# Performance work log

Measured on AMD Instinct MI355X. Metric: run time of the kernel, lower is better.

## Reference

```python
import jax, jax.numpy as jnp
import numpy as np

HIDDEN = 2048
N_HEADS = 16
N_KV_HEADS = 8
HEAD_DIM = 128
ROTARY_DIM = 32  # int(128 * 0.25), already even
ROPE_THETA = 10000000.0
EPS = 1e-6
BATCH, SEQ = 2, 2048


def _rmsnorm(x, w, eps=EPS):
    # per-head RMSNorm over last dim; weight is zero-init, scale = 1 + w
    r = jax.lax.rsqrt(jnp.mean(x * x, axis=-1, keepdims=True) + eps)
    return x * r * (1.0 + w)


def _rope(x, positions, rotary_dim, theta):
    # x: [b, s, h, rotary_dim]; rotate-halves RoPE
    half = rotary_dim // 2
    inv_freq = 1.0 / (theta ** (jnp.arange(half, dtype=jnp.float32) / half))
    ang = positions.astype(jnp.float32)[:, :, None] * inv_freq  # [b, s, half]
    cos = jnp.cos(ang)[:, :, None, :]
    sin = jnp.sin(ang)[:, :, None, :]
    x1, x2 = x[..., :half], x[..., half:]
    return jnp.concatenate([x1 * cos - x2 * sin, x1 * sin + x2 * cos], axis=-1)


def setup_inputs() -> dict:
    key = jax.random.key(0)
    ks = jax.random.split(key, 8)
    scale = lambda fan_in: 1.0 / np.sqrt(fan_in)
    x = jax.random.normal(ks[0], (BATCH, SEQ, HIDDEN), dtype=jnp.float32)
    Wq = jax.random.normal(ks[1], (HIDDEN, N_HEADS * HEAD_DIM * 2), jnp.float32) * scale(HIDDEN)
    Wk = jax.random.normal(ks[2], (HIDDEN, N_KV_HEADS * HEAD_DIM), jnp.float32) * scale(HIDDEN)
    Wv = jax.random.normal(ks[3], (HIDDEN, N_KV_HEADS * HEAD_DIM), jnp.float32) * scale(HIDDEN)
    Wo = jax.random.normal(ks[4], (N_HEADS * HEAD_DIM, HIDDEN), jnp.float32) * scale(N_HEADS * HEAD_DIM)
    q_norm_w = jax.random.normal(ks[5], (HEAD_DIM,), jnp.float32) * 0.02
    k_norm_w = jax.random.normal(ks[6], (HEAD_DIM,), jnp.float32) * 0.02
    attention_mask = jnp.ones((BATCH, SEQ), dtype=jnp.int32)
    positions = jnp.broadcast_to(jnp.arange(SEQ, dtype=jnp.int32), (BATCH, SEQ))
    return {"x": x, "attention_mask": attention_mask, "positions": positions,
            "Wq": Wq, "Wk": Wk, "Wv": Wv, "Wo": Wo,
            "q_norm_w": q_norm_w, "k_norm_w": k_norm_w}


def reference(x, attention_mask, positions, Wq, Wk, Wv, Wo, q_norm_w, k_norm_w):
    b, s, _ = x.shape
    g = N_HEADS // N_KV_HEADS  # GQA group size

    q_all = jnp.einsum('bsh,ho->bso', x, Wq).reshape(b, s, N_HEADS, HEAD_DIM * 2)
    q, gate = jnp.split(q_all, 2, axis=-1)          # each [b,s,H,D]
    gate = gate.reshape(b, s, N_HEADS * HEAD_DIM)
    q = _rmsnorm(q, q_norm_w)
    k = _rmsnorm(jnp.einsum('bsh,ho->bso', x, Wk).reshape(b, s, N_KV_HEADS, HEAD_DIM), k_norm_w)
    v = jnp.einsum('bsh,ho->bso', x, Wv).reshape(b, s, N_KV_HEADS, HEAD_DIM)

    # partial RoPE on first ROTARY_DIM dims
    q = jnp.concatenate([_rope(q[..., :ROTARY_DIM], positions, ROTARY_DIM, ROPE_THETA), q[..., ROTARY_DIM:]], axis=-1)
    k = jnp.concatenate([_rope(k[..., :ROTARY_DIM], positions, ROTARY_DIM, ROPE_THETA), k[..., ROTARY_DIM:]], axis=-1)

    # grouped-query causal attention
    qg = q.reshape(b, s, N_KV_HEADS, g, HEAD_DIM)
    scores = jnp.einsum('bqhgd,bkhd->bhgqk', qg, k) / jnp.sqrt(jnp.float32(HEAD_DIM))
    causal = jnp.tril(jnp.ones((s, s), dtype=bool))
    key_valid = attention_mask.astype(bool)[:, None, None, None, :]  # [b,1,1,1,k]
    mask = causal[None, None, None, :, :] & key_valid
    scores = jnp.where(mask, scores, jnp.finfo(scores.dtype).min)
    probs = jax.nn.softmax(scores, axis=-1)
    attn = jnp.einsum('bhgqk,bkhd->bqhgd', probs, v).reshape(b, s, N_HEADS * HEAD_DIM)

    attn = attn * jax.nn.sigmoid(gate)
    return jnp.einsum('bso,oh->bsh', attn, Wo)
```

## Files before the change

### kernel.cpp

```cpp
#include <hip/hip_runtime.h>
#include <cstdint>

typedef __bf16  bf16;
typedef __bf16  bf16x8 __attribute__((ext_vector_type(8)));
typedef __bf16  bf16x4 __attribute__((ext_vector_type(4)));
typedef float   f32x4  __attribute__((ext_vector_type(4)));

#define GLOAD_LDS16(g, l) __builtin_amdgcn_global_load_lds( \
    (const __attribute__((address_space(1))) void*)(g),     \
    (__attribute__((address_space(3))) void*)(l), 16, 0, 0)

#define SEQ   2048
#define HID   2048
#define NH    16
#define NKV   8
#define HD    128
#define NQKV  6144
#define MTOT  4096

__global__ __launch_bounds__(256) void convx(const float* __restrict__ x, bf16* __restrict__ xb) {
    int i = blockIdx.x * 256 + threadIdx.x;
    f32x4 v = ((const f32x4*)x)[i];
    bf16x4 o;
    o[0] = (bf16)v[0]; o[1] = (bf16)v[1]; o[2] = (bf16)v[2]; o[3] = (bf16)v[3];
    ((bf16x4*)xb)[i] = o;
}

__global__ __launch_bounds__(256) void transw(const float* __restrict__ W, bf16* __restrict__ WT, int N) {
    int n0 = blockIdx.x * 64, k0 = blockIdx.y * 64;
    __shared__ float tile[64][65];
    int t = threadIdx.x;
    int tn = t & 63, t4 = t >> 6;
    #pragma unroll
    for (int i = 0; i < 16; ++i) {
        int kk = i * 4 + t4;
        tile[kk][tn] = W[(size_t)(k0 + kk) * N + n0 + tn];
    }
    __syncthreads();
    #pragma unroll
    for (int i = 0; i < 16; ++i) {
        int nn = i * 4 + t4;
        WT[(size_t)(n0 + nn) * HID + k0 + tn] = (bf16)tile[tn][nn];
    }
}

template<bool OUT_BF16>
__global__ __launch_bounds__(256) void gemm_bt(const bf16* __restrict__ A, const bf16* __restrict__ Bt,
                                               void* __restrict__ C, int M, int N, int K) {
    __shared__ __align__(16) bf16 As[128 * 32];
    __shared__ __align__(16) bf16 Bs[128 * 32];
    const int tid = threadIdx.x;
    const int wave = tid >> 6, lane = tid & 63;
    const int quad = lane >> 4, cl = lane & 15;
    const int tile_n = blockIdx.x * 128, tile_m = blockIdx.y * 128;
    const int wm = (wave & 1) * 64, wn = (wave >> 1) * 64;
    f32x4 acc[4][4] = {};

    for (int k0 = 0; k0 < K; k0 += 32) {
        #pragma unroll
        for (int j = 0; j < 2; ++j) {
            int c = (j * 4 + wave) * 64 + lane;
            int row = c >> 2, kq = c & 3;
            GLOAD_LDS16(A  + (size_t)(tile_m + row) * K + k0 + kq * 8, As + (size_t)(j * 4 + wave) * 512);
            GLOAD_LDS16(Bt + (size_t)(tile_n + row) * K + k0 + kq * 8, Bs + (size_t)(j * 4 + wave) * 512);
        }
        __syncthreads();
        bf16x8 a[4], b[4];
        #pragma unroll
        for (int t = 0; t < 4; ++t) {
            a[t] = *(const bf16x8*)(As + (wm + t * 16 + cl) * 32 + quad * 8);
            b[t] = *(const bf16x8*)(Bs + (wn + t * 16 + cl) * 32 + quad * 8);
        }
        #pragma unroll
        for (int mt = 0; mt < 4; ++mt)
            #pragma unroll
            for (int nt = 0; nt < 4; ++nt)
                acc[mt][nt] = __builtin_amdgcn_mfma_f32_16x16x32_bf16(a[mt], b[nt], acc[mt][nt], 0, 0, 0);
        __syncthreads();
    }
    #pragma unroll
    for (int mt = 0; mt < 4; ++mt)
        #pragma unroll
        for (int nt = 0; nt < 4; ++nt)
            #pragma unroll
            for (int r = 0; r < 4; ++r) {
                int row = tile_m + wm + mt * 16 + quad * 4 + r;
                int col = tile_n + wn + nt * 16 + cl;
                float v = acc[mt][nt][r];
                if (OUT_BF16) ((bf16*)C)[(size_t)row * N + col] = (bf16)v;
                else          ((float*)C)[(size_t)row * N + col] = v;
            }
}

__global__ __launch_bounds__(256) void qk_post(const bf16* __restrict__ qkv,
                                               const float* __restrict__ qnw, const float* __restrict__ knw,
                                               const int* __restrict__ positions,
                                               bf16* __restrict__ Qh, bf16* __restrict__ Kh) {
    int tk = blockIdx.x;
    int b = tk >> 11, s = tk & 2047;
    int wave = threadIdx.x >> 6, lane = threadIdx.x & 63;
    float pos = (float)positions[tk];
    int fi = lane & 15;
    float ang = pos * exp2f(-(float)fi * 1.4533435415278355f);
    float cv = cosf(ang), sv = sinf(ang);

    #pragma unroll
    for (int i = 0; i < 4; ++i) {
        int h = wave + i * 4;
        const bf16* base = qkv + (size_t)tk * NQKV + h * 256;
        float v0 = (float)base[lane], v1 = (float)base[lane + 64];
        float ssq = v0 * v0 + v1 * v1;
        #pragma unroll
        for (int off = 32; off; off >>= 1) ssq += __shfl_xor(ssq, off);
        float rn = rsqrtf(ssq * (1.0f / 128.0f) + 1e-6f);
        float q0 = v0 * rn * (1.0f + qnw[lane]);
        float q1 = v1 * rn * (1.0f + qnw[lane + 64]);
        float other = __shfl_xor(q0, 16);
        float q0r = q0;
        if (lane < 16)      q0r = q0 * cv - other * sv;
        else if (lane < 32) q0r = other * sv + q0 * cv;
        bf16* qout = Qh + ((size_t)(b * NH + h) * SEQ + s) * HD;
        qout[lane] = (bf16)q0r; qout[lane + 64] = (bf16)q1;
    }
    #pragma unroll
    for (int i = 0; i < 2; ++i) {
        int h = wave + i * 4;
        const bf16* base = qkv + (size_t)tk * NQKV + 4096 + h * HD;
        float v0 = (float)base[lane], v1 = (float)base[lane + 64];
        float ssq = v0 * v0 + v1 * v1;
        #pragma unroll
        for (int off = 32; off; off >>= 1) ssq += __shfl_xor(ssq, off);
        float rn = rsqrtf(ssq * (1.0f / 128.0f) + 1e-6f);
        float k0 = v0 * rn * (1.0f + knw[lane]);
        float k1 = v1 * rn * (1.0f + knw[lane + 64]);
        float other = __shfl_xor(k0, 16);
        float k0r = k0;
        if (lane < 16)      k0r = k0 * cv - other * sv;
        else if (lane < 32) k0r = other * sv + k0 * cv;
        bf16* kout = Kh + ((size_t)(b * NKV + h) * SEQ + s) * HD;
        kout[lane] = (bf16)k0r; kout[lane + 64] = (bf16)k1;
    }
}

__global__ __launch_bounds__(256) void vtrans(const bf16* __restrict__ qkv, bf16* __restrict__ VT) {
    int bh = blockIdx.x >> 5;
    int st = blockIdx.x & 31;
    int b = bh >> 3, h = bh & 7;
    __shared__ float tile[64][129];
    int t = threadIdx.x;
    const bf16* src = qkv + ((size_t)(b * SEQ) + st * 64) * NQKV + 5120 + h * HD;
    #pragma unroll
    for (int i = 0; i < 32; ++i) {
        int idx = i * 256 + t;
        int tok = idx >> 7, d = idx & 127;
        tile[tok][d] = (float)src[(size_t)tok * NQKV + d];
    }
    __syncthreads();
    bf16* dst = VT + (size_t)(b * NKV + h) * HD * SEQ + st * 64;
    #pragma unroll
    for (int i = 0; i < 32; ++i) {
        int idx = i * 256 + t;
        int d = idx >> 6, sx = idx & 63;
        dst[(size_t)d * SEQ + sx] = (bf16)tile[sx][d];
    }
}

__global__ __launch_bounds__(256, 4) void attn_kernel(const bf16* __restrict__ Qh, const bf16* __restrict__ Kh,
                                                      const bf16* __restrict__ VT, const bf16* __restrict__ qkv,
                                                      const int* __restrict__ amask, bf16* __restrict__ attnb) {
    const int bx = blockIdx.x;
    const int hb = bx >> 5;
    const int head = hb & 15, b = hb >> 4;
    const int qt = ((bx & 31) + hb) & 31;
    const int kvh = head >> 1;
    __shared__ __align__(16) bf16 Ks[64 * 128];
    __shared__ __align__(16) bf16 Vs[128 * 64];
    __shared__ __align__(16) bf16 Ps[4 * 16 * 64];
    const int tid = threadIdx.x, wave = tid >> 6, lane = tid & 63;
    const int quad = lane >> 4, cl = lane & 15;

    const bf16* qsrc = Qh + ((size_t)(b * NH + head) * SEQ + qt * 64) * HD;
    bf16x8 aq[4];
    #pragma unroll
    for (int kc = 0; kc < 4; ++kc)
        aq[kc] = *(const bf16x8*)(qsrc + (size_t)(wave * 16 + cl) * HD + kc * 32 + quad * 8);

    float mstate[4], lstate[4];
    f32x4 oacc[8] = {};
    #pragma unroll
    for (int r = 0; r < 4; ++r) { mstate[r] = -1e30f; lstate[r] = 0.0f; }
    const int qrow_glob = qt * 64 + wave * 16 + quad * 4;
    const float scale = 0.08838834764831845f;

    for (int kt = 0; kt <= qt; ++kt) {
        __syncthreads();
        const bf16* ksrc = Kh + ((size_t)(b * NKV + kvh) * SEQ + kt * 64) * HD;
        const bf16* vsrc = VT + (size_t)(b * NKV + kvh) * HD * SEQ + kt * 64;
        #pragma unroll
        for (int j = 0; j < 4; ++j) {
            int s = (j * 4 + wave) * 64 + lane;
            int rK = s >> 4, cK = s & 15;
            GLOAD_LDS16(ksrc + (size_t)rK * HD + ((cK ^ (rK & 15)) << 3), Ks + (size_t)s * 8);
            int dV = s >> 3, cV = s & 7;
            GLOAD_LDS16(vsrc + (size_t)dV * SEQ + ((cV ^ (dV & 7)) << 3), Vs + (size_t)s * 8);
        }
        __syncthreads();

        f32x4 sc[4] = {};
        #pragma unroll
        for (int nt = 0; nt < 4; ++nt)
            #pragma unroll
            for (int kc = 0; kc < 4; ++kc) {
                bf16x8 bk = *(const bf16x8*)(Ks + (size_t)(nt * 16 + cl) * 128 + (((kc * 4 + quad) ^ cl) << 3));
                sc[nt] = __builtin_amdgcn_mfma_f32_16x16x32_bf16(aq[kc], bk, sc[nt], 0, 0, 0);
            }

        bool colok[4];
        int kcolb[4];
        #pragma unroll
        for (int nt = 0; nt < 4; ++nt) {
            kcolb[nt] = kt * 64 + nt * 16 + cl;
            colok[nt] = (amask[b * SEQ + kcolb[nt]] != 0);
        }

        float alpha[4];
        #pragma unroll
        for (int r = 0; r < 4; ++r) {
            float rv[4];
            float tmax = -1e30f;
            #pragma unroll
            for (int nt = 0; nt < 4; ++nt) {
                float v = sc[nt][r] * scale;
                bool ok = colok[nt] && (kcolb[nt] <= qrow_glob + r);
                v = ok ? v : -1e30f;
                rv[nt] = v;
                tmax = fmaxf(tmax, v);
            }
            #pragma unroll
            for (int off = 8; off; off >>= 1) tmax = fmaxf(tmax, __shfl_xor(tmax, off));
            float mnew = fmaxf(mstate[r], tmax);
            float al = __expf(mstate[r] - mnew);
            mstate[r] = mnew; alpha[r] = al;
            float rsum = 0.0f;
            int prow = quad * 4 + r;
            #pragma unroll
            for (int nt = 0; nt < 4; ++nt) {
                float p = __expf(rv[nt] - mnew);
                rsum += p;
                Ps[wave * 1024 + prow * 64 + ((nt * 16 + cl) ^ (quad << 4))] = (bf16)p;
            }
            #pragma unroll
            for (int off = 8; off; off >>= 1) rsum += __shfl_xor(rsum, off);
            lstate[r] = lstate[r] * al + rsum;
        }
        #pragma unroll
        for (int n2 = 0; n2 < 8; ++n2)
            #pragma unroll
            for (int r = 0; r < 4; ++r) oacc[n2][r] *= alpha[r];

        bf16x8 ap[2];
        #pragma unroll
        for (int c = 0; c < 2; ++c)
            ap[c] = *(const bf16x8*)(Ps + wave * 1024 + cl * 64 + ((c * 32 + quad * 8) ^ ((cl >> 2) << 4)));
        #pragma unroll
        for (int n2 = 0; n2 < 8; ++n2)
            #pragma unroll
            for (int c = 0; c < 2; ++c) {
                bf16x8 bv = *(const bf16x8*)(Vs + (size_t)(n2 * 16 + cl) * 64 + (((c * 4 + quad) ^ (cl & 7)) << 3));
                oacc[n2] = __builtin_amdgcn_mfma_f32_16x16x32_bf16(ap[c], bv, oacc[n2], 0, 0, 0);
            }
    }

    #pragma unroll
    for (int r = 0; r < 4; ++r) {
        int srow = qt * 64 + wave * 16 + quad * 4 + r;
        float linv = 1.0f / lstate[r];
        #pragma unroll
        for (int n2 = 0; n2 < 8; ++n2) {
            int d = n2 * 16 + cl;
            float g = (float)qkv[(size_t)(b * SEQ + srow) * NQKV + head * 256 + 128 + d];
            float sig = 1.0f / (1.0f + __expf(-g));
            float v = oacc[n2][r] * linv * sig;
            attnb[(size_t)(b * SEQ + srow) * HID + head * HD + d] = (bf16)v;
        }
    }
}

extern "C" void kernel_launch(void* const* d_in, const int* in_sizes, int n_in,
                              void* d_out, int out_size, void* d_ws, size_t ws_size,
                              hipStream_t stream) {
    const float* x        = (const float*)d_in[0];
    const int*   amask    = (const int*)d_in[1];
    const int*   positions= (const int*)d_in[2];
    const float* Wq       = (const float*)d_in[3];
    const float* Wk       = (const float*)d_in[4];
    const float* Wv       = (const float*)d_in[5];
    const float* Wo       = (const float*)d_in[6];
    const float* qnw      = (const float*)d_in[7];
    const float* knw      = (const float*)d_in[8];
    float* out = (float*)d_out;
    char* ws = (char*)d_ws;

    bf16* xb    = (bf16*)(ws);
    bf16* wqkvT = (bf16*)(ws + 16777216);
    bf16* woT   = (bf16*)(ws + 41943040);
    bf16* qkv   = (bf16*)(ws + 50331648);
    bf16* Qh    = (bf16*)(ws + 100663296);
    bf16* Kh    = (bf16*)(ws + 117440512);
    bf16* VT    = (bf16*)(ws + 125829120);
    bf16* attnb = (bf16*)(ws + 134217728);

    convx<<<8192, 256, 0, stream>>>(x, xb);
    transw<<<dim3(64, 32), 256, 0, stream>>>(Wq, wqkvT, 4096);
    transw<<<dim3(16, 32), 256, 0, stream>>>(Wk, wqkvT + (size_t)4096 * HID, 1024);
    transw<<<dim3(16, 32), 256, 0, stream>>>(Wv, wqkvT + (size_t)5120 * HID, 1024);
    transw<<<dim3(32, 32), 256, 0, stream>>>(Wo, woT, 2048);

    gemm_bt<true><<<dim3(48, 32), 256, 0, stream>>>(xb, wqkvT, qkv, MTOT, NQKV, HID);
    qk_post<<<4096, 256, 0, stream>>>(qkv, qnw, knw, positions, Qh, Kh);
    vtrans<<<512, 256, 0, stream>>>(qkv, VT);
    attn_kernel<<<1024, 256, 0, stream>>>(Qh, Kh, VT, qkv, amask, attnb);
    gemm_bt<false><<<dim3(16, 32), 256, 0, stream>>>(attnb, woT, out, MTOT, HID, HID);

    (void)in_sizes; (void)n_in; (void)out_size; (void)ws_size;
}
```

Baseline: 484.5 us.

## Merge prep and post kernels, use 32x32 MFMA in GEMM, exp2 softmax

Fuses the input conversion and four weight-transpose launches into one prep kernel, and the QK norm/RoPE and V-transpose into one post kernel, to cut launch overhead and tail gaps. The GEMM switches from 16x16x32 to 32x32x16 MFMA tiles, which need fewer LDS fragment loads per FLOP. The attention softmax folds log2(e) into the scale and uses exp2f, and applies the causal comparison only on the diagonal tile. The GEMM output write pattern changes to match the 32x32 accumulator layout.

```diff
diff --git a/kernel.cpp b/kernel.cpp
--- a/kernel.cpp
+++ b/kernel.cpp
@@ -5,6 +5,7 @@
 typedef __bf16  bf16x8 __attribute__((ext_vector_type(8)));
 typedef __bf16  bf16x4 __attribute__((ext_vector_type(4)));
 typedef float   f32x4  __attribute__((ext_vector_type(4)));
+typedef float   f32x16 __attribute__((ext_vector_type(16)));
 
 #define GLOAD_LDS16(g, l) __builtin_amdgcn_global_load_lds( \
     (const __attribute__((address_space(1))) void*)(g),     \
@@ -18,18 +19,9 @@
 #define NQKV  6144
 #define MTOT  4096
 
-__global__ __launch_bounds__(256) void convx(const float* __restrict__ x, bf16* __restrict__ xb) {
-    int i = blockIdx.x * 256 + threadIdx.x;
-    f32x4 v = ((const f32x4*)x)[i];
-    bf16x4 o;
-    o[0] = (bf16)v[0]; o[1] = (bf16)v[1]; o[2] = (bf16)v[2]; o[3] = (bf16)v[3];
-    ((bf16x4*)xb)[i] = o;
-}
-
-__global__ __launch_bounds__(256) void transw(const float* __restrict__ W, bf16* __restrict__ WT, int N) {
-    int n0 = blockIdx.x * 64, k0 = blockIdx.y * 64;
+__device__ __forceinline__ void transw_body(const float* __restrict__ W, bf16* __restrict__ WT,
+                                            int N, int n0, int k0, int t) {
     __shared__ float tile[64][65];
-    int t = threadIdx.x;
     int tn = t & 63, t4 = t >> 6;
     #pragma unroll
     for (int i = 0; i < 16; ++i) {
@@ -41,6 +33,32 @@
     for (int i = 0; i < 16; ++i) {
         int nn = i * 4 + t4;
         WT[(size_t)(n0 + nn) * HID + k0 + tn] = (bf16)tile[tn][nn];
+    }
+}
+
+__global__ __launch_bounds__(256) void prep_kernel(const float* __restrict__ x, bf16* __restrict__ xb,
+                                                   const float* __restrict__ Wq, const float* __restrict__ Wk,
+                                                   const float* __restrict__ Wv, const float* __restrict__ Wo,
+                                                   bf16* __restrict__ wqkvT, bf16* __restrict__ woT) {
+    int bx = blockIdx.x, t = threadIdx.x;
+    if (bx < 8192) {
+        int i = bx * 256 + t;
+        f32x4 v = ((const f32x4*)x)[i];
+        bf16x4 o;
+        o[0] = (bf16)v[0]; o[1] = (bf16)v[1]; o[2] = (bf16)v[2]; o[3] = (bf16)v[3];
+        ((bf16x4*)xb)[i] = o;
+    } else if (bx < 8192 + 2048) {
+        int idx = bx - 8192;
+        transw_body(Wq, wqkvT, 4096, (idx & 63) * 64, (idx >> 6) * 64, t);
+    } else if (bx < 8192 + 2048 + 512) {
+        int idx = bx - (8192 + 2048);
+        transw_body(Wk, wqkvT + (size_t)4096 * HID, 1024, (idx & 15) * 64, (idx >> 4) * 64, t);
+    } else if (bx < 8192 + 2048 + 1024) {
+        int idx = bx - (8192 + 2048 + 512);
+        transw_body(Wv, wqkvT + (size_t)5120 * HID, 1024, (idx & 15) * 64, (idx >> 4) * 64, t);
+    } else {
+        int idx = bx - (8192 + 2048 + 1024);
+        transw_body(Wo, woT, 2048, (idx & 31) * 64, (idx >> 5) * 64, t);
     }
 }
 
@@ -51,10 +69,10 @@
     __shared__ __align__(16) bf16 Bs[128 * 32];
     const int tid = threadIdx.x;
     const int wave = tid >> 6, lane = tid & 63;
-    const int quad = lane >> 4, cl = lane & 15;
+    const int l31 = lane & 31, half = lane >> 5;
     const int tile_n = blockIdx.x * 128, tile_m = blockIdx.y * 128;
     const int wm = (wave & 1) * 64, wn = (wave >> 1) * 64;
-    f32x4 acc[4][4] = {};
+    f32x16 acc[2][2] = {};
 
     for (int k0 = 0; k0 < K; k0 += 32) {
         #pragma unroll
@@ -65,103 +83,109 @@
             GLOAD_LDS16(Bt + (size_t)(tile_n + row) * K + k0 + kq * 8, Bs + (size_t)(j * 4 + wave) * 512);
         }
         __syncthreads();
-        bf16x8 a[4], b[4];
-        #pragma unroll
-        for (int t = 0; t < 4; ++t) {
-            a[t] = *(const bf16x8*)(As + (wm + t * 16 + cl) * 32 + quad * 8);
-            b[t] = *(const bf16x8*)(Bs + (wn + t * 16 + cl) * 32 + quad * 8);
-        }
-        #pragma unroll
-        for (int mt = 0; mt < 4; ++mt)
-            #pragma unroll
-            for (int nt = 0; nt < 4; ++nt)
-                acc[mt][nt] = __builtin_amdgcn_mfma_f32_16x16x32_bf16(a[mt], b[nt], acc[mt][nt], 0, 0, 0);
-        __syncthreads();
-    }
-    #pragma unroll
-    for (int mt = 0; mt < 4; ++mt)
-        #pragma unroll
-        for (int nt = 0; nt < 4; ++nt)
-            #pragma unroll
-            for (int r = 0; r < 4; ++r) {
-                int row = tile_m + wm + mt * 16 + quad * 4 + r;
-                int col = tile_n + wn + nt * 16 + cl;
-                float v = acc[mt][nt][r];
+        bf16x8 a[2][2], b[2][2];
+        #pragma unroll
+        for (int mt = 0; mt < 2; ++mt)
+            #pragma unroll
+            for (int kh = 0; kh < 2; ++kh) {
+                a[mt][kh] = *(const bf16x8*)(As + (size_t)(wm + mt * 32 + l31) * 32 + kh * 16 + half * 8);
+                b[mt][kh] = *(const bf16x8*)(Bs + (size_t)(wn + mt * 32 + l31) * 32 + kh * 16 + half * 8);
+            }
+        #pragma unroll
+        for (int mt = 0; mt < 2; ++mt)
+            #pragma unroll
+            for (int nt = 0; nt < 2; ++nt)
+                #pragma unroll
+                for (int kh = 0; kh < 2; ++kh)
+                    acc[mt][nt] = __builtin_amdgcn_mfma_f32_32x32x16_bf16(a[mt][kh], b[nt][kh], acc[mt][nt], 0, 0, 0);
+        __syncthreads();
+    }
+    #pragma unroll
+    for (int mt = 0; mt < 2; ++mt)
+        #pragma unroll
+        for (int nt = 0; nt < 2; ++nt)
+            #pragma unroll
+            for (int reg = 0; reg < 16; ++reg) {
+                int row = tile_m + wm + mt * 32 + (reg & 3) + ((reg >> 2) * 8) + half * 4;
+                int col = tile_n + wn + nt * 32 + l31;
+                float v = acc[mt][nt][reg];
                 if (OUT_BF16) ((bf16*)C)[(size_t)row * N + col] = (bf16)v;
                 else          ((float*)C)[(size_t)row * N + col] = v;
             }
 }
 
-__global__ __launch_bounds__(256) void qk_post(const bf16* __restrict__ qkv,
-                                               const float* __restrict__ qnw, const float* __restrict__ knw,
-                                               const int* __restrict__ positions,
-                                               bf16* __restrict__ Qh, bf16* __restrict__ Kh) {
-    int tk = blockIdx.x;
-    int b = tk >> 11, s = tk & 2047;
-    int wave = threadIdx.x >> 6, lane = threadIdx.x & 63;
-    float pos = (float)positions[tk];
-    int fi = lane & 15;
-    float ang = pos * exp2f(-(float)fi * 1.4533435415278355f);
-    float cv = cosf(ang), sv = sinf(ang);
-
-    #pragma unroll
-    for (int i = 0; i < 4; ++i) {
-        int h = wave + i * 4;
-        const bf16* base = qkv + (size_t)tk * NQKV + h * 256;
-        float v0 = (float)base[lane], v1 = (float)base[lane + 64];
-        float ssq = v0 * v0 + v1 * v1;
-        #pragma unroll
-        for (int off = 32; off; off >>= 1) ssq += __shfl_xor(ssq, off);
-        float rn = rsqrtf(ssq * (1.0f / 128.0f) + 1e-6f);
-        float q0 = v0 * rn * (1.0f + qnw[lane]);
-        float q1 = v1 * rn * (1.0f + qnw[lane + 64]);
-        float other = __shfl_xor(q0, 16);
-        float q0r = q0;
-        if (lane < 16)      q0r = q0 * cv - other * sv;
-        else if (lane < 32) q0r = other * sv + q0 * cv;
-        bf16* qout = Qh + ((size_t)(b * NH + h) * SEQ + s) * HD;
-        qout[lane] = (bf16)q0r; qout[lane + 64] = (bf16)q1;
-    }
-    #pragma unroll
-    for (int i = 0; i < 2; ++i) {
-        int h = wave + i * 4;
-        const bf16* base = qkv + (size_t)tk * NQKV + 4096 + h * HD;
-        float v0 = (float)base[lane], v1 = (float)base[lane + 64];
-        float ssq = v0 * v0 + v1 * v1;
-        #pragma unroll
-        for (int off = 32; off; off >>= 1) ssq += __shfl_xor(ssq, off);
-        float rn = rsqrtf(ssq * (1.0f / 128.0f) + 1e-6f);
-        float k0 = v0 * rn * (1.0f + knw[lane]);
-        float k1 = v1 * rn * (1.0f + knw[lane + 64]);
-        float other = __shfl_xor(k0, 16);
-        float k0r = k0;
-        if (lane < 16)      k0r = k0 * cv - other * sv;
-        else if (lane < 32) k0r = other * sv + k0 * cv;
-        bf16* kout = Kh + ((size_t)(b * NKV + h) * SEQ + s) * HD;
-        kout[lane] = (bf16)k0r; kout[lane + 64] = (bf16)k1;
-    }
-}
-
-__global__ __launch_bounds__(256) void vtrans(const bf16* __restrict__ qkv, bf16* __restrict__ VT) {
-    int bh = blockIdx.x >> 5;
-    int st = blockIdx.x & 31;
-    int b = bh >> 3, h = bh & 7;
-    __shared__ float tile[64][129];
-    int t = threadIdx.x;
-    const bf16* src = qkv + ((size_t)(b * SEQ) + st * 64) * NQKV + 5120 + h * HD;
-    #pragma unroll
-    for (int i = 0; i < 32; ++i) {
-        int idx = i * 256 + t;
-        int tok = idx >> 7, d = idx & 127;
-        tile[tok][d] = (float)src[(size_t)tok * NQKV + d];
-    }
-    __syncthreads();
-    bf16* dst = VT + (size_t)(b * NKV + h) * HD * SEQ + st * 64;
-    #pragma unroll
-    for (int i = 0; i < 32; ++i) {
-        int idx = i * 256 + t;
-        int d = idx >> 6, sx = idx & 63;
-        dst[(size_t)d * SEQ + sx] = (bf16)tile[sx][d];
+__global__ __launch_bounds__(256) void post_kernel(const bf16* __restrict__ qkv,
+                                                   const float* __restrict__ qnw, const float* __restrict__ knw,
+                                                   const int* __restrict__ positions,
+                                                   bf16* __restrict__ Qh, bf16* __restrict__ Kh,
+                                                   bf16* __restrict__ VT) {
+    int bx = blockIdx.x;
+    if (bx < 4096) {
+        int tk = bx;
+        int b = tk >> 11, s = tk & 2047;
+        int wave = threadIdx.x >> 6, lane = threadIdx.x & 63;
+        float pos = (float)positions[tk];
+        int fi = lane & 15;
+        float ang = pos * exp2f(-(float)fi * 1.4533435415278355f);
+        float cv = cosf(ang), sv = sinf(ang);
+
+        #pragma unroll
+        for (int i = 0; i < 4; ++i) {
+            int h = wave + i * 4;
+            const bf16* base = qkv + (size_t)tk * NQKV + h * 256;
+            float v0 = (float)base[lane], v1 = (float)base[lane + 64];
+            float ssq = v0 * v0 + v1 * v1;
+            #pragma unroll
+            for (int off = 32; off; off >>= 1) ssq += __shfl_xor(ssq, off);
+            float rn = rsqrtf(ssq * (1.0f / 128.0f) + 1e-6f);
+            float q0 = v0 * rn * (1.0f + qnw[lane]);
+            float q1 = v1 * rn * (1.0f + qnw[lane + 64]);
+            float other = __shfl_xor(q0, 16);
+            float q0r = q0;
+            if (lane < 16)      q0r = q0 * cv - other * sv;
+            else if (lane < 32) q0r = other * sv + q0 * cv;
+            bf16* qout = Qh + ((size_t)(b * NH + h) * SEQ + s) * HD;
+            qout[lane] = (bf16)q0r; qout[lane + 64] = (bf16)q1;
+        }
+        #pragma unroll
+        for (int i = 0; i < 2; ++i) {
+            int h = wave + i * 4;
+            const bf16* base = qkv + (size_t)tk * NQKV + 4096 + h * HD;
+            float v0 = (float)base[lane], v1 = (float)base[lane + 64];
+            float ssq = v0 * v0 + v1 * v1;
+            #pragma unroll
+            for (int off = 32; off; off >>= 1) ssq += __shfl_xor(ssq, off);
+            float rn = rsqrtf(ssq * (1.0f / 128.0f) + 1e-6f);
+            float k0 = v0 * rn * (1.0f + knw[lane]);
+            float k1 = v1 * rn * (1.0f + knw[lane + 64]);
+            float other = __shfl_xor(k0, 16);
+            float k0r = k0;
+            if (lane < 16)      k0r = k0 * cv - other * sv;
+            else if (lane < 32) k0r = other * sv + k0 * cv;
+            bf16* kout = Kh + ((size_t)(b * NKV + h) * SEQ + s) * HD;
+            kout[lane] = (bf16)k0r; kout[lane + 64] = (bf16)k1;
+        }
+    } else {
+        int idx = bx - 4096;
+        int bh = idx >> 5, st = idx & 31;
+        int b = bh >> 3, h = bh & 7;
+        __shared__ float tile[64][129];
+        int t = threadIdx.x;
+        const bf16* src = qkv + ((size_t)(b * SEQ) + st * 64) * NQKV + 5120 + h * HD;
+        #pragma unroll
+        for (int i = 0; i < 32; ++i) {
+            int ii = i * 256 + t;
+            int tok = ii >> 7, d = ii & 127;
+            tile[tok][d] = (float)src[(size_t)tok * NQKV + d];
+        }
+        __syncthreads();
+        bf16* dst = VT + (size_t)(b * NKV + h) * HD * SEQ + st * 64;
+        #pragma unroll
+        for (int i = 0; i < 32; ++i) {
+            int ii = i * 256 + t;
+            int d = ii >> 6, sx = ii & 63;
+            dst[(size_t)d * SEQ + sx] = (bf16)tile[sx][d];
+        }
     }
 }
 
@@ -190,7 +214,7 @@
     #pragma unroll
     for (int r = 0; r < 4; ++r) { mstate[r] = -1e30f; lstate[r] = 0.0f; }
     const int qrow_glob = qt * 64 + wave * 16 + quad * 4;
-    const float scale = 0.08838834764831845f;
+    const float scale = 0.08838834764831845f * 1.4426950408889634f;
 
     for (int kt = 0; kt <= qt; ++kt) {
         __syncthreads();
@@ -222,6 +246,7 @@
             kcolb[nt] = kt * 64 + nt * 16 + cl;
             colok[nt] = (amask[b * SEQ + kcolb[nt]] != 0);
         }
+        const bool diag = (kt == qt);
 
         float alpha[4];
         #pragma unroll
@@ -231,7 +256,7 @@
             #pragma unroll
             for (int nt = 0; nt < 4; ++nt) {
                 float v = sc[nt][r] * scale;
-                bool ok = colok[nt] && (kcolb[nt] <= qrow_glob + r);
+                bool ok = colok[nt] && (!diag || (kcolb[nt] <= qrow_glob + r));
                 v = ok ? v : -1e30f;
                 rv[nt] = v;
                 tmax = fmaxf(tmax, v);
@@ -239,13 +264,13 @@
             #pragma unroll
             for (int off = 8; off; off >>= 1) tmax = fmaxf(tmax, __shfl_xor(tmax, off));
             float mnew = fmaxf(mstate[r], tmax);
-            float al = __expf(mstate[r] - mnew);
+            float al = exp2f(mstate[r] - mnew);
             mstate[r] = mnew; alpha[r] = al;
             float rsum = 0.0f;
             int prow = quad * 4 + r;
             #pragma unroll
             for (int nt = 0; nt < 4; ++nt) {
-                float p = __expf(rv[nt] - mnew);
+                float p = exp2f(rv[nt] - mnew);
                 rsum += p;
                 Ps[wave * 1024 + prow * 64 + ((nt * 16 + cl) ^ (quad << 4))] = (bf16)p;
             }
@@ -310,15 +335,9 @@
     bf16* VT    = (bf16*)(ws + 125829120);
     bf16* attnb = (bf16*)(ws + 134217728);
 
-    convx<<<8192, 256, 0, stream>>>(x, xb);
-    transw<<<dim3(64, 32), 256, 0, stream>>>(Wq, wqkvT, 4096);
-    transw<<<dim3(16, 32), 256, 0, stream>>>(Wk, wqkvT + (size_t)4096 * HID, 1024);
-    transw<<<dim3(16, 32), 256, 0, stream>>>(Wv, wqkvT + (size_t)5120 * HID, 1024);
-    transw<<<dim3(32, 32), 256, 0, stream>>>(Wo, woT, 2048);
-
+    prep_kernel<<<12288, 256, 0, stream>>>(x, xb, Wq, Wk, Wv, Wo, wqkvT, woT);
     gemm_bt<true><<<dim3(48, 32), 256, 0, stream>>>(xb, wqkvT, qkv, MTOT, NQKV, HID);
-    qk_post<<<4096, 256, 0, stream>>>(qkv, qnw, knw, positions, Qh, Kh);
-    vtrans<<<512, 256, 0, stream>>>(qkv, VT);
+    post_kernel<<<4608, 256, 0, stream>>>(qkv, qnw, knw, positions, Qh, Kh, VT);
     attn_kernel<<<1024, 256, 0, stream>>>(Qh, Kh, VT, qkv, amask, attnb);
     gemm_bt<false><<<dim3(16, 32), 256, 0, stream>>>(attnb, woT, out, MTOT, HID, HID);
 
```

Result: no change. 481.4 us (-0.6%).
